# Kernel tuning notes

Measured on AMD Instinct MI355X. Metric: run time of the kernel, lower is better.

The kernel has to match this reference:

```python
import jax, jax.numpy as jnp
import numpy as np

INPUT_DIM = 1024
HIDDEN_DIM = 512
SEQ_LEN = 512


def setup_inputs() -> dict:
    key = jax.random.key(0)
    ks = jax.random.split(key, 7)
    s = 1.0 / np.sqrt(INPUT_DIM)
    s2 = 1.0 / np.sqrt(HIDDEN_DIM)
    return {
        "vectors": jax.random.normal(ks[0], (1, SEQ_LEN, INPUT_DIM), dtype=jnp.float32),
        "W_h": jax.random.uniform(ks[1], (HIDDEN_DIM, INPUT_DIM), jnp.float32, -s, s),
        "b_h": jax.random.uniform(ks[2], (HIDDEN_DIM,), jnp.float32, -s, s),
        "W_m": jax.random.uniform(ks[3], (HIDDEN_DIM, INPUT_DIM), jnp.float32, -s, s),
        "b_m": jax.random.uniform(ks[4], (HIDDEN_DIM,), jnp.float32, -s, s),
        "w2": jax.random.uniform(ks[5], (HIDDEN_DIM,), jnp.float32, -s2, s2),
        "b2": jax.random.uniform(ks[6], (), jnp.float32, -s2, s2),
    }


def reference(vectors, W_h, b_h, W_m, b_m, w2, b2):
    # vectors: [1, S, D] -> squeeze leading batch dim (matches torch .squeeze(0))
    x = vectors[0]  # [S, D]
    # Two batched GEMMs replacing the per-token Python loop
    H = x @ W_h.T + b_h  # [S, Hd] head representations
    M = x @ W_m.T + b_m  # [S, Hd] modifier representations
    # Pairwise broadcast add + tanh + dot with layer_2 weights -> [S, S] scores
    pair = jnp.tanh(H[:, None, :] + M[None, :, :])  # [S, S, Hd]
    scores = jnp.einsum('hmd,d->hm', pair, w2) + b2
    return scores
```

## Files before the change

kernel.cpp:

```cpp
#include <hip/hip_runtime.h>

#define C2 2.8853900817779268f
#define DIN 1024
#define HD 512

typedef short short8 __attribute__((ext_vector_type(8)));
typedef float floatx4 __attribute__((ext_vector_type(4)));

__device__ __forceinline__ float rcp_fast(float x){ return __builtin_amdgcn_rcpf(x); }
__device__ __forceinline__ float exp2_fast(float x){ return __builtin_amdgcn_exp2f(x); }
__device__ __forceinline__ float comp4(const float4& v, int i){
    return i==0 ? v.x : i==1 ? v.y : i==2 ? v.z : v.w;
}
__device__ __forceinline__ unsigned short f2bf(float f){
    union{float f; unsigned int u;} v; v.f = f;
    unsigned int u = v.u;
    return (unsigned short)((u + 0x7FFFu + ((u >> 16) & 1u)) >> 16);
}

__global__ __launch_bounds__(256) void convert_kernel(
    const float* __restrict__ x, const float* __restrict__ Wh,
    const float* __restrict__ Wm, unsigned short* __restrict__ xb,
    unsigned short* __restrict__ whb, unsigned short* __restrict__ wmb)
{
    int r = blockIdx.z;
    const float* s = r == 0 ? x : r == 1 ? Wh : Wm;
    unsigned short* d = r == 0 ? xb : r == 1 ? whb : wmb;
    int i = (blockIdx.x * 256 + threadIdx.x) * 4;
    float4 v = *(const float4*)(s + i);
    ushort4 o = { f2bf(v.x), f2bf(v.y), f2bf(v.z), f2bf(v.w) };
    *(ushort4*)(d + i) = o;
}

__global__ __launch_bounds__(256) void mfma_gemm_kernel(
    const unsigned short* __restrict__ xb, const unsigned short* __restrict__ whb,
    const unsigned short* __restrict__ wmb, const float* __restrict__ bh,
    const float* __restrict__ bm, float* __restrict__ EH, float* __restrict__ EM)
{
    int mat = blockIdx.z;
    const unsigned short* B = mat ? wmb : whb;
    const float* bias = mat ? bm : bh;
    float* O = mat ? EM : EH;
    int j0 = blockIdx.x * 32, s0 = blockIdx.y * 32;
    int wave = threadIdx.x >> 6, lane = threadIdx.x & 63;
    int sw = (wave & 1) * 16, jw = (wave >> 1) * 16;
    int m = lane & 15, quad = lane >> 4;

    const unsigned short* ap = xb + (size_t)(s0 + sw + m) * DIN + quad * 8;
    const unsigned short* bp = B  + (size_t)(j0 + jw + m) * DIN + quad * 8;

    floatx4 acc = {0.f, 0.f, 0.f, 0.f};
    #pragma unroll 8
    for (int k = 0; k < DIN; k += 32){
        short8 af = *(const short8*)(ap + k);
        short8 bf = *(const short8*)(bp + k);
        acc = __builtin_amdgcn_mfma_f32_16x16x32_bf16(af, bf, acc, 0, 0, 0);
    }
    int col = j0 + jw + m;
    float bv = bias[col];
    #pragma unroll
    for (int i = 0; i < 4; i++){
        int row = s0 + sw + quad * 4 + i;
        O[(size_t)row * HD + col] = exp2_fast(C2 * (acc[i] + bv));
    }
}

__global__ __launch_bounds__(256, 4) void scores_kernel(
    const float* __restrict__ EH, const float* __restrict__ EM,
    const float* __restrict__ w2, float* __restrict__ Q)
{
    int m0 = blockIdx.x * 64, h0 = blockIdx.y * 32, d0 = blockIdx.z * 64;
    __shared__ float Hs[32 * 68];
    __shared__ float Ms[64 * 68];
    __shared__ float wsS[64];
    int tid = threadIdx.x;
    int tx = tid & 15, ty = tid >> 4;
    #pragma unroll
    for (int l = 0; l < 2; l++){
        int slot = tid + 256 * l;
        int row = slot >> 4, q = slot & 15;
        float4 h = *(const float4*)(EH + (size_t)(h0 + row) * HD + d0 + q * 4);
        *(float4*)&Hs[row * 68 + q * 4] = h;
    }
    #pragma unroll
    for (int l = 0; l < 4; l++){
        int slot = tid + 256 * l;
        int mm = slot >> 4, q = slot & 15;
        float4 v = *(const float4*)(EM + (size_t)(m0 + mm) * HD + d0 + q * 4);
        Ms[(q*4 + 0) * 68 + mm] = v.x;
        Ms[(q*4 + 1) * 68 + mm] = v.y;
        Ms[(q*4 + 2) * 68 + mm] = v.z;
        Ms[(q*4 + 3) * 68 + mm] = v.w;
    }
    if (tid < 16){
        float4 w = *(const float4*)(w2 + d0 + tid * 4);
        float4 ws = {-2.f * w.x, -2.f * w.y, -2.f * w.z, -2.f * w.w};
        *(float4*)&wsS[tid * 4] = ws;
    }
    __syncthreads();

    float acc[2][4] = {};
    #pragma unroll 2
    for (int it = 0; it < 16; it++){
        int dk = it * 4;
        float4 w4 = *(const float4*)&wsS[dk];
        float4 hA = *(const float4*)&Hs[(ty*2 + 0) * 68 + dk];
        float4 hB = *(const float4*)&Hs[(ty*2 + 1) * 68 + dk];
        #pragma unroll
        for (int dd = 0; dd < 4; dd++){
            float4 mv = *(const float4*)&Ms[(dk + dd) * 68 + tx * 4];
            float w = comp4(w4, dd);
            float e0 = comp4(hA, dd), e1 = comp4(hB, dd);
            acc[0][0] = fmaf(w, rcp_fast(fmaf(e0, mv.x, 1.f)), acc[0][0]);
            acc[0][1] = fmaf(w, rcp_fast(fmaf(e0, mv.y, 1.f)), acc[0][1]);
            acc[0][2] = fmaf(w, rcp_fast(fmaf(e0, mv.z, 1.f)), acc[0][2]);
            acc[0][3] = fmaf(w, rcp_fast(fmaf(e0, mv.w, 1.f)), acc[0][3]);
            acc[1][0] = fmaf(w, rcp_fast(fmaf(e1, mv.x, 1.f)), acc[1][0]);
            acc[1][1] = fmaf(w, rcp_fast(fmaf(e1, mv.y, 1.f)), acc[1][1]);
            acc[1][2] = fmaf(w, rcp_fast(fmaf(e1, mv.z, 1.f)), acc[1][2]);
            acc[1][3] = fmaf(w, rcp_fast(fmaf(e1, mv.w, 1.f)), acc[1][3]);
        }
    }
    float* Qp = Q + (size_t)blockIdx.z * 262144;
    #pragma unroll
    for (int i = 0; i < 2; i++){
        float4 v = {acc[i][0], acc[i][1], acc[i][2], acc[i][3]};
        *(float4*)&Qp[(h0 + ty*2 + i) * 512 + m0 + tx * 4] = v;
    }
}

__global__ __launch_bounds__(256) void combine_kernel(
    const float* __restrict__ Q, const float* __restrict__ w2,
    const float* __restrict__ b2, float* __restrict__ out)
{
    int tid = threadIdx.x;
    __shared__ float red[4];
    __shared__ float c0s;
    float s = 0.f;
    if (tid < 128){ float4 v = ((const float4*)w2)[tid]; s = v.x + v.y + v.z + v.w; }
    #pragma unroll
    for (int off = 32; off; off >>= 1) s += __shfl_down(s, off, 64);
    if (tid < 128 && (tid & 63) == 0) red[tid >> 6] = s;
    __syncthreads();
    if (tid == 0) c0s = red[0] + red[1] + b2[0];
    __syncthreads();
    float c0 = c0s;
    int g = blockIdx.x * 256 + tid;
    const float4* Q4 = (const float4*)Q;
    float4 a = Q4[g];
    #pragma unroll
    for (int sl = 1; sl < 8; sl++){
        float4 b = Q4[sl * 65536 + g];
        a.x += b.x; a.y += b.y; a.z += b.z; a.w += b.w;
    }
    float4 o = {a.x + c0, a.y + c0, a.z + c0, a.w + c0};
    ((float4*)out)[g] = o;
}

extern "C" void kernel_launch(void* const* d_in, const int* in_sizes, int n_in,
                              void* d_out, int out_size, void* d_ws, size_t ws_size,
                              hipStream_t stream) {
    const float* x   = (const float*)d_in[0];
    const float* Wh  = (const float*)d_in[1];
    const float* bh  = (const float*)d_in[2];
    const float* Wm  = (const float*)d_in[3];
    const float* bm  = (const float*)d_in[4];
    const float* w2  = (const float*)d_in[5];
    const float* b2  = (const float*)d_in[6];
    float* out = (float*)d_out;
    (void)in_sizes; (void)n_in; (void)out_size; (void)ws_size;

    float* w = (float*)d_ws;
    unsigned short* xb  = (unsigned short*)(w);
    unsigned short* whb = (unsigned short*)(w + 262144);
    unsigned short* wmb = (unsigned short*)(w + 524288);
    float* EH = w + 786432;
    float* EM = w + 1048576;
    float* Q  = w + 1310720;

    convert_kernel<<<dim3(512, 1, 3), 256, 0, stream>>>(x, Wh, Wm, xb, whb, wmb);
    mfma_gemm_kernel<<<dim3(16, 16, 2), 256, 0, stream>>>(xb, whb, wmb, bh, bm, EH, EM);
    scores_kernel<<<dim3(8, 16, 8), 256, 0, stream>>>(EH, EM, w2, Q);
    combine_kernel<<<256, 256, 0, stream>>>(Q, w2, b2, out);
}
```

Baseline: 108.6 us.

## Combine four reciprocals into one via common denominator; store EM transposed

The scores inner loop now sums four w/den terms with a single reciprocal of the product of the four denominators. This trades four rcp ops for several extra multiplies and FMAs on the transcendental-bound path. The GEMM also writes the modifier matrix transposed, so the scores kernel can load it into shared memory with float4 stores instead of scattered scalar stores. The product of four denominators of the form 1+e^{2h}e^{2m} can overflow fp32 for large activations, which is a precision risk.

```diff
diff --git a/kernel.cpp b/kernel.cpp
--- a/kernel.cpp
+++ b/kernel.cpp
@@ -35,12 +35,11 @@
 __global__ __launch_bounds__(256) void mfma_gemm_kernel(
     const unsigned short* __restrict__ xb, const unsigned short* __restrict__ whb,
     const unsigned short* __restrict__ wmb, const float* __restrict__ bh,
-    const float* __restrict__ bm, float* __restrict__ EH, float* __restrict__ EM)
+    const float* __restrict__ bm, float* __restrict__ EH, float* __restrict__ EMT)
 {
     int mat = blockIdx.z;
     const unsigned short* B = mat ? wmb : whb;
     const float* bias = mat ? bm : bh;
-    float* O = mat ? EM : EH;
     int j0 = blockIdx.x * 32, s0 = blockIdx.y * 32;
     int wave = threadIdx.x >> 6, lane = threadIdx.x & 63;
     int sw = (wave & 1) * 16, jw = (wave >> 1) * 16;
@@ -58,15 +57,21 @@
     }
     int col = j0 + jw + m;
     float bv = bias[col];
-    #pragma unroll
-    for (int i = 0; i < 4; i++){
-        int row = s0 + sw + quad * 4 + i;
-        O[(size_t)row * HD + col] = exp2_fast(C2 * (acc[i] + bv));
+    if (mat == 0){
+        #pragma unroll
+        for (int i = 0; i < 4; i++){
+            int row = s0 + sw + quad * 4 + i;
+            EH[(size_t)row * HD + col] = exp2_fast(C2 * (acc[i] + bv));
+        }
+    } else {
+        float4 v = { exp2_fast(C2 * (acc[0] + bv)), exp2_fast(C2 * (acc[1] + bv)),
+                     exp2_fast(C2 * (acc[2] + bv)), exp2_fast(C2 * (acc[3] + bv)) };
+        *(float4*)&EMT[(size_t)col * 512 + s0 + sw + quad * 4] = v;
     }
 }
 
 __global__ __launch_bounds__(256, 4) void scores_kernel(
-    const float* __restrict__ EH, const float* __restrict__ EM,
+    const float* __restrict__ EH, const float* __restrict__ EMT,
     const float* __restrict__ w2, float* __restrict__ Q)
 {
     int m0 = blockIdx.x * 64, h0 = blockIdx.y * 32, d0 = blockIdx.z * 64;
@@ -79,18 +84,15 @@
     for (int l = 0; l < 2; l++){
         int slot = tid + 256 * l;
         int row = slot >> 4, q = slot & 15;
-        float4 h = *(const float4*)(EH + (size_t)(h0 + row) * HD + d0 + q * 4);
-        *(float4*)&Hs[row * 68 + q * 4] = h;
+        *(float4*)&Hs[row * 68 + q * 4] =
+            *(const float4*)(EH + (size_t)(h0 + row) * HD + d0 + q * 4);
     }
     #pragma unroll
     for (int l = 0; l < 4; l++){
         int slot = tid + 256 * l;
-        int mm = slot >> 4, q = slot & 15;
-        float4 v = *(const float4*)(EM + (size_t)(m0 + mm) * HD + d0 + q * 4);
-        Ms[(q*4 + 0) * 68 + mm] = v.x;
-        Ms[(q*4 + 1) * 68 + mm] = v.y;
-        Ms[(q*4 + 2) * 68 + mm] = v.z;
-        Ms[(q*4 + 3) * 68 + mm] = v.w;
+        int dd = slot >> 4, q = slot & 15;
+        *(float4*)&Ms[dd * 68 + q * 4] =
+            *(const float4*)(EMT + (size_t)(d0 + dd) * 512 + m0 + q * 4);
     }
     if (tid < 16){
         float4 w = *(const float4*)(w2 + d0 + tid * 4);
@@ -103,22 +105,29 @@
     #pragma unroll 2
     for (int it = 0; it < 16; it++){
         int dk = it * 4;
-        float4 w4 = *(const float4*)&wsS[dk];
-        float4 hA = *(const float4*)&Hs[(ty*2 + 0) * 68 + dk];
-        float4 hB = *(const float4*)&Hs[(ty*2 + 1) * 68 + dk];
+        float4 w4  = *(const float4*)&wsS[dk];
+        float4 hA  = *(const float4*)&Hs[(ty*2 + 0) * 68 + dk];
+        float4 hB  = *(const float4*)&Hs[(ty*2 + 1) * 68 + dk];
+        float4 mv0 = *(const float4*)&Ms[(dk + 0) * 68 + tx * 4];
+        float4 mv1 = *(const float4*)&Ms[(dk + 1) * 68 + tx * 4];
+        float4 mv2 = *(const float4*)&Ms[(dk + 2) * 68 + tx * 4];
+        float4 mv3 = *(const float4*)&Ms[(dk + 3) * 68 + tx * 4];
         #pragma unroll
-        for (int dd = 0; dd < 4; dd++){
-            float4 mv = *(const float4*)&Ms[(dk + dd) * 68 + tx * 4];
-            float w = comp4(w4, dd);
-            float e0 = comp4(hA, dd), e1 = comp4(hB, dd);
-            acc[0][0] = fmaf(w, rcp_fast(fmaf(e0, mv.x, 1.f)), acc[0][0]);
-            acc[0][1] = fmaf(w, rcp_fast(fmaf(e0, mv.y, 1.f)), acc[0][1]);
-            acc[0][2] = fmaf(w, rcp_fast(fmaf(e0, mv.z, 1.f)), acc[0][2]);
-            acc[0][3] = fmaf(w, rcp_fast(fmaf(e0, mv.w, 1.f)), acc[0][3]);
-            acc[1][0] = fmaf(w, rcp_fast(fmaf(e1, mv.x, 1.f)), acc[1][0]);
-            acc[1][1] = fmaf(w, rcp_fast(fmaf(e1, mv.y, 1.f)), acc[1][1]);
-            acc[1][2] = fmaf(w, rcp_fast(fmaf(e1, mv.z, 1.f)), acc[1][2]);
-            acc[1][3] = fmaf(w, rcp_fast(fmaf(e1, mv.w, 1.f)), acc[1][3]);
+        for (int hh = 0; hh < 2; hh++){
+            float4 hv = hh ? hB : hA;
+            #pragma unroll
+            for (int j = 0; j < 4; j++){
+                float den0 = fmaf(hv.x, comp4(mv0, j), 1.f);
+                float den1 = fmaf(hv.y, comp4(mv1, j), 1.f);
+                float den2 = fmaf(hv.z, comp4(mv2, j), 1.f);
+                float den3 = fmaf(hv.w, comp4(mv3, j), 1.f);
+                float p01 = den0 * den1;
+                float p23 = den2 * den3;
+                float t1 = fmaf(w4.y, den0, w4.x * den1);
+                float t2 = fmaf(w4.w, den2, w4.z * den3);
+                float N  = fmaf(t2, p01, t1 * p23);
+                acc[hh][j] = fmaf(N, rcp_fast(p01 * p23), acc[hh][j]);
+            }
         }
     }
     float* Qp = Q + (size_t)blockIdx.z * 262144;
@@ -174,12 +183,12 @@
     unsigned short* xb  = (unsigned short*)(w);
     unsigned short* whb = (unsigned short*)(w + 262144);
     unsigned short* wmb = (unsigned short*)(w + 524288);
-    float* EH = w + 786432;
-    float* EM = w + 1048576;
-    float* Q  = w + 1310720;
+    float* EH  = w + 786432;
+    float* EMT = w + 1048576;
+    float* Q   = w + 1310720;
 
     convert_kernel<<<dim3(512, 1, 3), 256, 0, stream>>>(x, Wh, Wm, xb, whb, wmb);
-    mfma_gemm_kernel<<<dim3(16, 16, 2), 256, 0, stream>>>(xb, whb, wmb, bh, bm, EH, EM);
-    scores_kernel<<<dim3(8, 16, 8), 256, 0, stream>>>(EH, EM, w2, Q);
+    mfma_gemm_kernel<<<dim3(16, 16, 2), 256, 0, stream>>>(xb, whb, wmb, bh, bm, EH, EMT);
+    scores_kernel<<<dim3(8, 16, 8), 256, 0, stream>>>(EH, EMT, w2, Q);
     combine_kernel<<<256, 256, 0, stream>>>(Q, w2, b2, out);
 }
```

After: 103.8 us. 4.4% less time.

## Merge four tanh reciprocals into one and drop split-D combine pass

Applied to the files above, without the earlier changes.

The scores kernel now runs the whole hidden dimension in each block, using double-buffered shared-memory tiles of 16x16 outputs with one output per thread. This writes the final scores directly and removes the partial-sum buffer and the separate combine kernel. Four w/(1+e_h*e_m) terms are combined algebraically into one fraction, so a single fast reciprocal replaces four. The bias constant from the w2 sum plus b2 is now computed inside the convert kernel. In exchange there is less register-level reuse, more LDS reads per output, and a risk of fp32 overflow in the product of four denominators when activations are large.

```diff
diff --git a/kernel.cpp b/kernel.cpp
--- a/kernel.cpp
+++ b/kernel.cpp
@@ -9,9 +9,6 @@
 
 __device__ __forceinline__ float rcp_fast(float x){ return __builtin_amdgcn_rcpf(x); }
 __device__ __forceinline__ float exp2_fast(float x){ return __builtin_amdgcn_exp2f(x); }
-__device__ __forceinline__ float comp4(const float4& v, int i){
-    return i==0 ? v.x : i==1 ? v.y : i==2 ? v.z : v.w;
-}
 __device__ __forceinline__ unsigned short f2bf(float f){
     union{float f; unsigned int u;} v; v.f = f;
     unsigned int u = v.u;
@@ -20,16 +17,30 @@
 
 __global__ __launch_bounds__(256) void convert_kernel(
     const float* __restrict__ x, const float* __restrict__ Wh,
-    const float* __restrict__ Wm, unsigned short* __restrict__ xb,
-    unsigned short* __restrict__ whb, unsigned short* __restrict__ wmb)
+    const float* __restrict__ Wm, const float* __restrict__ w2,
+    const float* __restrict__ b2, unsigned short* __restrict__ xb,
+    unsigned short* __restrict__ whb, unsigned short* __restrict__ wmb,
+    float* __restrict__ c0out)
 {
     int r = blockIdx.z;
     const float* s = r == 0 ? x : r == 1 ? Wh : Wm;
     unsigned short* d = r == 0 ? xb : r == 1 ? whb : wmb;
-    int i = (blockIdx.x * 256 + threadIdx.x) * 4;
+    int tid = threadIdx.x;
+    int i = (blockIdx.x * 256 + tid) * 4;
     float4 v = *(const float4*)(s + i);
     ushort4 o = { f2bf(v.x), f2bf(v.y), f2bf(v.z), f2bf(v.w) };
     *(ushort4*)(d + i) = o;
+
+    if (blockIdx.z == 2 && blockIdx.x == 0){
+        __shared__ float red[2];
+        float sum = 0.f;
+        if (tid < 128){ float4 w = ((const float4*)w2)[tid]; sum = w.x + w.y + w.z + w.w; }
+        #pragma unroll
+        for (int off = 32; off; off >>= 1) sum += __shfl_down(sum, off, 64);
+        if (tid < 128 && (tid & 63) == 0) red[tid >> 6] = sum;
+        __syncthreads();
+        if (tid == 0) c0out[0] = red[0] + red[1] + b2[0];
+    }
 }
 
 __global__ __launch_bounds__(256) void mfma_gemm_kernel(
@@ -67,94 +78,74 @@
 
 __global__ __launch_bounds__(256, 4) void scores_kernel(
     const float* __restrict__ EH, const float* __restrict__ EM,
-    const float* __restrict__ w2, float* __restrict__ Q)
+    const float* __restrict__ w2, const float* __restrict__ c0p,
+    float* __restrict__ out)
 {
-    int m0 = blockIdx.x * 64, h0 = blockIdx.y * 32, d0 = blockIdx.z * 64;
-    __shared__ float Hs[32 * 68];
-    __shared__ float Ms[64 * 68];
-    __shared__ float wsS[64];
+    int m0 = blockIdx.x * 16, h0 = blockIdx.y * 16;
+    __shared__ float Hs[2][16 * 68];
+    __shared__ float Ms[2][16 * 68];
     int tid = threadIdx.x;
     int tx = tid & 15, ty = tid >> 4;
-    #pragma unroll
-    for (int l = 0; l < 2; l++){
-        int slot = tid + 256 * l;
-        int row = slot >> 4, q = slot & 15;
-        float4 h = *(const float4*)(EH + (size_t)(h0 + row) * HD + d0 + q * 4);
-        *(float4*)&Hs[row * 68 + q * 4] = h;
-    }
-    #pragma unroll
-    for (int l = 0; l < 4; l++){
-        int slot = tid + 256 * l;
-        int mm = slot >> 4, q = slot & 15;
-        float4 v = *(const float4*)(EM + (size_t)(m0 + mm) * HD + d0 + q * 4);
-        Ms[(q*4 + 0) * 68 + mm] = v.x;
-        Ms[(q*4 + 1) * 68 + mm] = v.y;
-        Ms[(q*4 + 2) * 68 + mm] = v.z;
-        Ms[(q*4 + 3) * 68 + mm] = v.w;
-    }
-    if (tid < 16){
-        float4 w = *(const float4*)(w2 + d0 + tid * 4);
-        float4 ws = {-2.f * w.x, -2.f * w.y, -2.f * w.z, -2.f * w.w};
-        *(float4*)&wsS[tid * 4] = ws;
-    }
+    const float* hp = EH + (size_t)(h0 + ty) * HD + tx * 4;
+    const float* mp = EM + (size_t)(m0 + ty) * HD + tx * 4;
+    int ldst = ty * 68 + tx * 4;
+
+    float4 hr = *(const float4*)hp;
+    float4 mr = *(const float4*)mp;
+    *(float4*)&Hs[0][ldst] = hr;
+    *(float4*)&Ms[0][ldst] = mr;
     __syncthreads();
 
-    float acc[2][4] = {};
-    #pragma unroll 2
-    for (int it = 0; it < 16; it++){
-        int dk = it * 4;
-        float4 w4 = *(const float4*)&wsS[dk];
-        float4 hA = *(const float4*)&Hs[(ty*2 + 0) * 68 + dk];
-        float4 hB = *(const float4*)&Hs[(ty*2 + 1) * 68 + dk];
+    float acc = 0.f;
+    for (int c = 0; c < 7; ++c){
+        hr = *(const float4*)(hp + (c + 1) * 64);
+        mr = *(const float4*)(mp + (c + 1) * 64);
+        const float* Hrow = &Hs[c & 1][ty * 68];
+        const float* Mrow = &Ms[c & 1][tx * 68];
+        const float* wc = w2 + c * 64;
         #pragma unroll
-        for (int dd = 0; dd < 4; dd++){
-            float4 mv = *(const float4*)&Ms[(dk + dd) * 68 + tx * 4];
-            float w = comp4(w4, dd);
-            float e0 = comp4(hA, dd), e1 = comp4(hB, dd);
-            acc[0][0] = fmaf(w, rcp_fast(fmaf(e0, mv.x, 1.f)), acc[0][0]);
-            acc[0][1] = fmaf(w, rcp_fast(fmaf(e0, mv.y, 1.f)), acc[0][1]);
-            acc[0][2] = fmaf(w, rcp_fast(fmaf(e0, mv.z, 1.f)), acc[0][2]);
-            acc[0][3] = fmaf(w, rcp_fast(fmaf(e0, mv.w, 1.f)), acc[0][3]);
-            acc[1][0] = fmaf(w, rcp_fast(fmaf(e1, mv.x, 1.f)), acc[1][0]);
-            acc[1][1] = fmaf(w, rcp_fast(fmaf(e1, mv.y, 1.f)), acc[1][1]);
-            acc[1][2] = fmaf(w, rcp_fast(fmaf(e1, mv.z, 1.f)), acc[1][2]);
-            acc[1][3] = fmaf(w, rcp_fast(fmaf(e1, mv.w, 1.f)), acc[1][3]);
+        for (int it = 0; it < 16; it++){
+            int dk = it * 4;
+            float4 hv = *(const float4*)(Hrow + dk);
+            float4 mv = *(const float4*)(Mrow + dk);
+            float w0 = wc[dk], w1 = wc[dk + 1], w2v = wc[dk + 2], w3 = wc[dk + 3];
+            float den0 = fmaf(hv.x, mv.x, 1.f);
+            float den1 = fmaf(hv.y, mv.y, 1.f);
+            float den2 = fmaf(hv.z, mv.z, 1.f);
+            float den3 = fmaf(hv.w, mv.w, 1.f);
+            float p01 = den0 * den1, p23 = den2 * den3;
+            float t1 = fmaf(w1, den0, w0 * den1);
+            float t2 = fmaf(w3, den2, w2v * den3);
+            float N  = fmaf(t2, p01, t1 * p23);
+            acc = fmaf(N, rcp_fast(p01 * p23), acc);
+        }
+        *(float4*)&Hs[(c + 1) & 1][ldst] = hr;
+        *(float4*)&Ms[(c + 1) & 1][ldst] = mr;
+        __syncthreads();
+    }
+    {
+        const float* Hrow = &Hs[1][ty * 68];
+        const float* Mrow = &Ms[1][tx * 68];
+        const float* wc = w2 + 7 * 64;
+        #pragma unroll
+        for (int it = 0; it < 16; it++){
+            int dk = it * 4;
+            float4 hv = *(const float4*)(Hrow + dk);
+            float4 mv = *(const float4*)(Mrow + dk);
+            float w0 = wc[dk], w1 = wc[dk + 1], w2v = wc[dk + 2], w3 = wc[dk + 3];
+            float den0 = fmaf(hv.x, mv.x, 1.f);
+            float den1 = fmaf(hv.y, mv.y, 1.f);
+            float den2 = fmaf(hv.z, mv.z, 1.f);
+            float den3 = fmaf(hv.w, mv.w, 1.f);
+            float p01 = den0 * den1, p23 = den2 * den3;
+            float t1 = fmaf(w1, den0, w0 * den1);
+            float t2 = fmaf(w3, den2, w2v * den3);
+            float N  = fmaf(t2, p01, t1 * p23);
+            acc = fmaf(N, rcp_fast(p01 * p23), acc);
         }
     }
-    float* Qp = Q + (size_t)blockIdx.z * 262144;
-    #pragma unroll
-    for (int i = 0; i < 2; i++){
-        float4 v = {acc[i][0], acc[i][1], acc[i][2], acc[i][3]};
-        *(float4*)&Qp[(h0 + ty*2 + i) * 512 + m0 + tx * 4] = v;
-    }
-}
-
-__global__ __launch_bounds__(256) void combine_kernel(
-    const float* __restrict__ Q, const float* __restrict__ w2,
-    const float* __restrict__ b2, float* __restrict__ out)
-{
-    int tid = threadIdx.x;
-    __shared__ float red[4];
-    __shared__ float c0s;
-    float s = 0.f;
-    if (tid < 128){ float4 v = ((const float4*)w2)[tid]; s = v.x + v.y + v.z + v.w; }
-    #pragma unroll
-    for (int off = 32; off; off >>= 1) s += __shfl_down(s, off, 64);
-    if (tid < 128 && (tid & 63) == 0) red[tid >> 6] = s;
-    __syncthreads();
-    if (tid == 0) c0s = red[0] + red[1] + b2[0];
-    __syncthreads();
-    float c0 = c0s;
-    int g = blockIdx.x * 256 + tid;
-    const float4* Q4 = (const float4*)Q;
-    float4 a = Q4[g];
-    #pragma unroll
-    for (int sl = 1; sl < 8; sl++){
-        float4 b = Q4[sl * 65536 + g];
-        a.x += b.x; a.y += b.y; a.z += b.z; a.w += b.w;
-    }
-    float4 o = {a.x + c0, a.y + c0, a.z + c0, a.w + c0};
-    ((float4*)out)[g] = o;
+    float c0 = c0p[0];
+    out[(size_t)(h0 + ty) * 512 + m0 + tx] = fmaf(-2.f, acc, c0);
 }
 
 extern "C" void kernel_launch(void* const* d_in, const int* in_sizes, int n_in,
@@ -176,10 +167,9 @@
     unsigned short* wmb = (unsigned short*)(w + 524288);
     float* EH = w + 786432;
     float* EM = w + 1048576;
-    float* Q  = w + 1310720;
+    float* c0 = w + 1310720;
 
-    convert_kernel<<<dim3(512, 1, 3), 256, 0, stream>>>(x, Wh, Wm, xb, whb, wmb);
+    convert_kernel<<<dim3(512, 1, 3), 256, 0, stream>>>(x, Wh, Wm, w2, b2, xb, whb, wmb, c0);
     mfma_gemm_kernel<<<dim3(16, 16, 2), 256, 0, stream>>>(xb, whb, wmb, bh, bm, EH, EM);
-    scores_kernel<<<dim3(8, 16, 8), 256, 0, stream>>>(EH, EM, w2, Q);
-    combine_kernel<<<256, 256, 0, stream>>>(Q, w2, b2, out);
+    scores_kernel<<<dim3(32, 32), 256, 0, stream>>>(EH, EM, w2, c0, out);
 }
```

Result: faster. 105.7 us (-2.7%).
